# Performance work log

Measured on AMD Instinct MI355X. Metric: run time of the kernel, lower is better.

The kernel has to match this reference:

```python
import jax, jax.numpy as jnp
import numpy as np


def _linear_params(key, fan_in, fan_out):
    # torch nn.Linear default init: U(-1/sqrt(fan_in), 1/sqrt(fan_in))
    kw, kb = jax.random.split(key)
    bound = 1.0 / np.sqrt(fan_in)
    W = jax.random.uniform(kw, (fan_out, fan_in), jnp.float32, -bound, bound)
    b = jax.random.uniform(kb, (fan_out,), jnp.float32, -bound, bound)
    return W, b


def setup_inputs() -> dict:
    key = jax.random.key(0)
    kx, k1, k7, k8, k9 = jax.random.split(key, 5)
    x = jax.random.normal(kx, (4194304, 6), dtype=jnp.float32)
    W1, b1 = _linear_params(k1, 6, 8)
    W7, b7 = _linear_params(k7, 8, 4)
    W8, b8 = _linear_params(k8, 4, 2)
    W9, b9 = _linear_params(k9, 2, 1)
    return {"x": x, "W1": W1, "b1": b1, "W7": W7, "b7": b7,
            "W8": W8, "b8": b8, "W9": W9, "b9": b9}


def reference(x, W1, b1, W7, b7, W8, b8, W9, b9):
    # forward only uses l1 -> relu -> l7 -> relu -> l8 -> relu -> l9 -> softplus
    z = jax.nn.relu(x @ W1.T + b1)      # [N, 8]
    z = jax.nn.relu(z @ W7.T + b7)      # [N, 4]
    z = jax.nn.relu(z @ W8.T + b8)      # [N, 2]
    z = z @ W9.T + b9                   # [N, 1]
    return jax.nn.softplus(z)
```

## Files before the change

kernel.cpp:

```cpp
#include <hip/hip_runtime.h>
#include <math.h>


__device__ __forceinline__ float softplus_f(float z) {
    return fmaxf(z, 0.0f) + log1pf(expf(-fabsf(z)));
}

__global__ __launch_bounds__(256) void encoder_mlp_kernel(
    const float* __restrict__ x,
    const float* __restrict__ W1, const float* __restrict__ b1,
    const float* __restrict__ W7, const float* __restrict__ b7,
    const float* __restrict__ W8, const float* __restrict__ b8,
    const float* __restrict__ W9, const float* __restrict__ b9,
    float* __restrict__ out, int n_rows)
{
    const int t = blockIdx.x * blockDim.x + threadIdx.x;
    const long long row0 = (long long)t * 4;
    if (row0 >= n_rows) return;

    float xr[4][6];
    bool full_quad = (row0 + 4 <= n_rows);

    if (full_quad) {
        const float4* xin = reinterpret_cast<const float4*>(x) + (size_t)t * 6;
        float4 v0 = xin[0], v1 = xin[1], v2 = xin[2],
               v3 = xin[3], v4 = xin[4], v5 = xin[5];
        xr[0][0] = v0.x; xr[0][1] = v0.y; xr[0][2] = v0.z; xr[0][3] = v0.w; xr[0][4] = v1.x; xr[0][5] = v1.y;
        xr[1][0] = v1.z; xr[1][1] = v1.w; xr[1][2] = v2.x; xr[1][3] = v2.y; xr[1][4] = v2.z; xr[1][5] = v2.w;
        xr[2][0] = v3.x; xr[2][1] = v3.y; xr[2][2] = v3.z; xr[2][3] = v3.w; xr[2][4] = v4.x; xr[2][5] = v4.y;
        xr[3][0] = v4.z; xr[3][1] = v4.w; xr[3][2] = v5.x; xr[3][3] = v5.y; xr[3][4] = v5.z; xr[3][5] = v5.w;
    } else {
        #pragma unroll
        for (int r = 0; r < 4; ++r) {
            long long row = row0 + r;
            #pragma unroll
            for (int k = 0; k < 6; ++k)
                xr[r][k] = (row < n_rows) ? x[row * 6 + k] : 0.0f;
        }
    }

    float res[4];
    #pragma unroll
    for (int r = 0; r < 4; ++r) {
        float h1[8];
        #pragma unroll
        for (int j = 0; j < 8; ++j) {
            float acc = b1[j];
            #pragma unroll
            for (int k = 0; k < 6; ++k) acc = fmaf(W1[j * 6 + k], xr[r][k], acc);
            h1[j] = fmaxf(acc, 0.0f);
        }
        float h7[4];
        #pragma unroll
        for (int j = 0; j < 4; ++j) {
            float acc = b7[j];
            #pragma unroll
            for (int k = 0; k < 8; ++k) acc = fmaf(W7[j * 8 + k], h1[k], acc);
            h7[j] = fmaxf(acc, 0.0f);
        }
        float h8[2];
        #pragma unroll
        for (int j = 0; j < 2; ++j) {
            float acc = b8[j];
            #pragma unroll
            for (int k = 0; k < 4; ++k) acc = fmaf(W8[j * 4 + k], h7[k], acc);
            h8[j] = fmaxf(acc, 0.0f);
        }
        float z = fmaf(W9[0], h8[0], fmaf(W9[1], h8[1], b9[0]));
        res[r] = softplus_f(z);
    }

    if (full_quad) {
        float4 o;
        o.x = res[0]; o.y = res[1]; o.z = res[2]; o.w = res[3];
        reinterpret_cast<float4*>(out)[t] = o;
    } else {
        #pragma unroll
        for (int r = 0; r < 4; ++r) {
            long long row = row0 + r;
            if (row < n_rows) out[row] = res[r];
        }
    }
}

extern "C" void kernel_launch(void* const* d_in, const int* in_sizes, int n_in,
                              void* d_out, int out_size, void* d_ws, size_t ws_size,
                              hipStream_t stream) {
    const float* x  = (const float*)d_in[0];
    const float* W1 = (const float*)d_in[1];
    const float* b1 = (const float*)d_in[2];
    const float* W7 = (const float*)d_in[3];
    const float* b7 = (const float*)d_in[4];
    const float* W8 = (const float*)d_in[5];
    const float* b8 = (const float*)d_in[6];
    const float* W9 = (const float*)d_in[7];
    const float* b9 = (const float*)d_in[8];
    float* out = (float*)d_out;

    const int n_rows = in_sizes[0] / 6;
    const int n_threads = (n_rows + 3) / 4;
    const int block = 256;
    const int grid = (n_threads + block - 1) / block;

    encoder_mlp_kernel<<<grid, block, 0, stream>>>(
        x, W1, b1, W7, b7, W8, b8, W9, b9, out, n_rows);
}
```

Baseline: 29.95 us.

## Pack row pairs into float2 vectors for packed FMA and use fast softplus

Rows are processed in pairs held as two-wide float vectors, so the compiler can emit packed FP32 math (v_pk_fma_f32) for the MLP layers. Softplus now uses the fast __expf/__logf intrinsics instead of the precise expf/log1pf, and the output goes out as a nontemporal store. The kernel is mostly bound by memory bandwidth (about 100 MB read), so cutting ALU work may have little effect. The fast log(1+e) loses some accuracy for tiny e.

```diff
diff --git a/kernel.cpp b/kernel.cpp
--- a/kernel.cpp
+++ b/kernel.cpp
@@ -2,8 +2,15 @@
 #include <math.h>
 
 
-__device__ __forceinline__ float softplus_f(float z) {
-    return fmaxf(z, 0.0f) + log1pf(expf(-fabsf(z)));
+typedef float v2f __attribute__((ext_vector_type(2)));
+typedef float v4f __attribute__((ext_vector_type(4)));
+
+__device__ __forceinline__ v2f vmax0(v2f a) {
+#if __has_builtin(__builtin_elementwise_max)
+    return __builtin_elementwise_max(a, (v2f)0.0f);
+#else
+    v2f r; r.x = fmaxf(a.x, 0.0f); r.y = fmaxf(a.y, 0.0f); return r;
+#endif
 }
 
 __global__ __launch_bounds__(256) void encoder_mlp_kernel(
@@ -18,62 +25,73 @@
     const long long row0 = (long long)t * 4;
     if (row0 >= n_rows) return;
 
-    float xr[4][6];
-    bool full_quad = (row0 + 4 <= n_rows);
+    const bool full_quad = (row0 + 4 <= n_rows);
+
+    v2f xp[2][6];
 
     if (full_quad) {
-        const float4* xin = reinterpret_cast<const float4*>(x) + (size_t)t * 6;
-        float4 v0 = xin[0], v1 = xin[1], v2 = xin[2],
-               v3 = xin[3], v4 = xin[4], v5 = xin[5];
-        xr[0][0] = v0.x; xr[0][1] = v0.y; xr[0][2] = v0.z; xr[0][3] = v0.w; xr[0][4] = v1.x; xr[0][5] = v1.y;
-        xr[1][0] = v1.z; xr[1][1] = v1.w; xr[1][2] = v2.x; xr[1][3] = v2.y; xr[1][4] = v2.z; xr[1][5] = v2.w;
-        xr[2][0] = v3.x; xr[2][1] = v3.y; xr[2][2] = v3.z; xr[2][3] = v3.w; xr[2][4] = v4.x; xr[2][5] = v4.y;
-        xr[3][0] = v4.z; xr[3][1] = v4.w; xr[3][2] = v5.x; xr[3][3] = v5.y; xr[3][4] = v5.z; xr[3][5] = v5.w;
+        const v4f* xin = reinterpret_cast<const v4f*>(x) + (size_t)t * 6;
+        v4f v0 = xin[0], v1 = xin[1], v2 = xin[2],
+            v3 = xin[3], v4 = xin[4], v5 = xin[5];
+        xp[0][0] = (v2f){v0.x, v1.z}; xp[0][1] = (v2f){v0.y, v1.w};
+        xp[0][2] = (v2f){v0.z, v2.x}; xp[0][3] = (v2f){v0.w, v2.y};
+        xp[0][4] = (v2f){v1.x, v2.z}; xp[0][5] = (v2f){v1.y, v2.w};
+        xp[1][0] = (v2f){v3.x, v4.z}; xp[1][1] = (v2f){v3.y, v4.w};
+        xp[1][2] = (v2f){v3.z, v5.x}; xp[1][3] = (v2f){v3.w, v5.y};
+        xp[1][4] = (v2f){v4.x, v5.z}; xp[1][5] = (v2f){v4.y, v5.w};
     } else {
         #pragma unroll
-        for (int r = 0; r < 4; ++r) {
-            long long row = row0 + r;
+        for (int p = 0; p < 2; ++p) {
             #pragma unroll
-            for (int k = 0; k < 6; ++k)
-                xr[r][k] = (row < n_rows) ? x[row * 6 + k] : 0.0f;
+            for (int k = 0; k < 6; ++k) {
+                long long ra = row0 + 2 * p, rb = ra + 1;
+                float a = (ra < n_rows) ? x[ra * 6 + k] : 0.0f;
+                float b = (rb < n_rows) ? x[rb * 6 + k] : 0.0f;
+                xp[p][k] = (v2f){a, b};
+            }
         }
     }
 
     float res[4];
     #pragma unroll
-    for (int r = 0; r < 4; ++r) {
-        float h1[8];
+    for (int p = 0; p < 2; ++p) {
+        v2f h1[8];
         #pragma unroll
         for (int j = 0; j < 8; ++j) {
-            float acc = b1[j];
+            v2f acc = (v2f)b1[j];
             #pragma unroll
-            for (int k = 0; k < 6; ++k) acc = fmaf(W1[j * 6 + k], xr[r][k], acc);
-            h1[j] = fmaxf(acc, 0.0f);
+            for (int k = 0; k < 6; ++k) acc += W1[j * 6 + k] * xp[p][k];
+            h1[j] = vmax0(acc);
         }
-        float h7[4];
+        v2f h7[4];
         #pragma unroll
         for (int j = 0; j < 4; ++j) {
-            float acc = b7[j];
+            v2f acc = (v2f)b7[j];
             #pragma unroll
-            for (int k = 0; k < 8; ++k) acc = fmaf(W7[j * 8 + k], h1[k], acc);
-            h7[j] = fmaxf(acc, 0.0f);
+            for (int k = 0; k < 8; ++k) acc += W7[j * 8 + k] * h1[k];
+            h7[j] = vmax0(acc);
         }
-        float h8[2];
+        v2f h8[2];
         #pragma unroll
         for (int j = 0; j < 2; ++j) {
-            float acc = b8[j];
+            v2f acc = (v2f)b8[j];
             #pragma unroll
-            for (int k = 0; k < 4; ++k) acc = fmaf(W8[j * 4 + k], h7[k], acc);
-            h8[j] = fmaxf(acc, 0.0f);
+            for (int k = 0; k < 4; ++k) acc += W8[j * 4 + k] * h7[k];
+            h8[j] = vmax0(acc);
         }
-        float z = fmaf(W9[0], h8[0], fmaf(W9[1], h8[1], b9[0]));
-        res[r] = softplus_f(z);
+        v2f z = W9[0] * h8[0] + W9[1] * h8[1] + (v2f)b9[0];
+        v2f az; az.x = fabsf(z.x); az.y = fabsf(z.y);
+        v2f e;  e.x = __expf(-az.x); e.y = __expf(-az.y);
+        v2f l;  l.x = __logf(1.0f + e.x); l.y = __logf(1.0f + e.y);
+        v2f r = vmax0(z) + l;
+        res[2 * p]     = r.x;
+        res[2 * p + 1] = r.y;
     }
 
     if (full_quad) {
-        float4 o;
+        v4f o;
         o.x = res[0]; o.y = res[1]; o.z = res[2]; o.w = res[3];
-        reinterpret_cast<float4*>(out)[t] = o;
+        __builtin_nontemporal_store(o, reinterpret_cast<v4f*>(out) + t);
     } else {
         #pragma unroll
         for (int r = 0; r < 4; ++r) {
```

New measurement: 26.97 us. 1.11x faster.
